# Kernel optimization log

Hardware: AMD Instinct MI355X
Metric: run time of the kernel (lower is better)

## Reference

```python
import jax, jax.numpy as jnp
import numpy as np

GRID_SIZE = 300


def setup_inputs() -> dict:
    key = jax.random.key(0)
    k1, k2 = jax.random.split(key)
    N, input_dim, out_dim = 2048, 256, 256
    x = jax.random.normal(k1, (N, input_dim), dtype=jnp.float32)
    scale = 1.0 / (np.sqrt(input_dim) * np.sqrt(GRID_SIZE))
    coeffs = jax.random.normal(k2, (2, out_dim, input_dim, GRID_SIZE), dtype=jnp.float32) * scale
    bias = jnp.zeros((1, out_dim), dtype=jnp.float32)
    return {"x": x, "coeffs": coeffs, "bias": bias}


def reference(x, coeffs, bias):
    # x: [N, I]; coeffs: [2, J, I, K]; bias: [1, J]
    grid_size = coeffs.shape[-1]
    k = jnp.arange(1, grid_size + 1, dtype=x.dtype)            # [K]
    ang = x[:, :, None] * k                                    # [N, I, K]
    c = jnp.cos(ang)
    s = jnp.sin(ang)
    # einsum('dbik,djik->bj') with d=2 split into cos/sin parts
    y = jnp.einsum('bik,jik->bj', c, coeffs[0]) + jnp.einsum('bik,jik->bj', s, coeffs[1])
    y = y + bias
    return y
```

## Files before the change

kernel.cpp:

```cpp
#include <hip/hip_runtime.h>
#include <stdint.h>

#define NB 2048
#define NI 256
#define NJ 256
#define GK 300
#define KPAD 320
#define KK_PER_I (2*KPAD)
#define NKC (NI*KK_PER_I/32)
#define CH_PER_I 20
#define SPLITK 32
#define II_PER_S (NI / SPLITK)
#define BM 128

#define B_BYTES  ((size_t)NKC * 16 * 1024)
#define P_BYTES  ((size_t)SPLITK * NB * NJ * 4)

typedef __bf16 bf16x8 __attribute__((ext_vector_type(8)));
typedef __bf16 bf16x2 __attribute__((ext_vector_type(2)));
typedef float  f32x4  __attribute__((ext_vector_type(4)));

__device__ __forceinline__ void sincos2pi(float ang, float& c, float& s) {
  float r = ang * 0.15915494309189535f;
  r = r - floorf(r);
  c = __builtin_amdgcn_cosf(r);
  s = __builtin_amdgcn_sinf(r);
}

__device__ __forceinline__ unsigned int pkbf(float c, float s) {
  bf16x2 p; p.x = (__bf16)c; p.y = (__bf16)s;
  return __builtin_bit_cast(unsigned int, p);
}

__device__ __forceinline__ void rot(float& c, float& s, float cr, float sr) {
  float nc = c * cr - s * sr;
  s = s * cr + c * sr;
  c = nc;
}

__global__ __launch_bounds__(256) void convert_b(const float* __restrict__ coeffs,
                                                 unsigned int* __restrict__ bw) {
  __shared__ uint4 sb[80][17];
  const int bid = blockIdx.x;
  const int i  = bid >> 4;
  const int jt = bid & 15;
  const int t  = (int)threadIdx.x;

  {
    const int jr = t >> 4;
    const int gq = t & 15;
    const int j  = jt * 16 + jr;
    const float4* r0 = (const float4*)(coeffs + (size_t)(j * NI + i) * GK);
    const float4* r1 = (const float4*)(coeffs + (size_t)((NJ + j) * NI + i) * GK);
    #pragma unroll
    for (int p = 0; p < 5; p++) {
      const int g = p * 16 + gq;
      uint4 w = {0u, 0u, 0u, 0u};
      if (g < GK / 4) {
        float4 a = r0[g];
        float4 b = r1[g];
        w.x = pkbf(a.x, b.x);
        w.y = pkbf(a.y, b.y);
        w.z = pkbf(a.z, b.z);
        w.w = pkbf(a.w, b.w);
      }
      sb[g][jr] = w;
    }
  }
  __syncthreads();
  {
    const int n  = t & 15;
    const int gl = t >> 4;
    #pragma unroll
    for (int p = 0; p < 5; p++) {
      const int g = p * 16 + gl;
      const int kc = i * 20 + (g >> 2);
      const unsigned int idx = ((unsigned int)(kc * 16 + jt) << 8) + ((g & 3) << 6) + (n << 2);
      *(uint4*)(bw + idx) = sb[g][n];
    }
  }
}

__global__ __launch_bounds__(256) void init_out(const float* __restrict__ bias,
                                                float* __restrict__ out) {
  const int tid = blockIdx.x * 256 + threadIdx.x;
  float4 b = ((const float4*)bias)[tid & 63];
  ((float4*)out)[tid] = b;
}

template <int MODE>
__global__ __launch_bounds__(256, 2) void fkan_gemm(const float* __restrict__ x,
                                                    const uint4* __restrict__ bw4,
                                                    float* __restrict__ dst) {
  const int bid  = blockIdx.x;
  const int virt = (bid & 7) * 64 + (bid >> 3);
  const int mt = virt & 15;
  const int s  = virt >> 4;
  const int m0 = mt * BM;

  const int t    = (int)threadIdx.x;
  const int lane = t & 63;
  const int wave = t >> 6;
  const int wr = wave >> 1;
  const int wc = wave & 1;
  const int q  = lane >> 4;
  const int ln = lane & 15;

  f32x4 acc[4][8];
  #pragma unroll
  for (int mm = 0; mm < 4; mm++)
    #pragma unroll
    for (int nn = 0; nn < 8; nn++)
      acc[mm][nn] = (f32x4){0.f, 0.f, 0.f, 0.f};

  const uint4* bptr = bw4 + (size_t)(wc * 8) * 64 + lane;

  int kc = s * (NKC / SPLITK);
  uint4 bcur[8], bnxt[8];
  #pragma unroll
  for (int nn = 0; nn < 8; nn++) bcur[nn] = bptr[(size_t)kc * 1024 + nn * 64];

  float stc[4], sts[4], c1a[4], s1a[4], cDa[4], sDa[4];

  #pragma unroll 1
  for (int ii = 0; ii < II_PER_S; ii++) {
    const int i = s * II_PER_S + ii;
    #pragma unroll
    for (int mm = 0; mm < 4; mm++) {
      const float xv = x[(m0 + wr * 64 + mm * 16 + ln) * NI + i];
      sincos2pi(xv, c1a[mm], s1a[mm]);
      sincos2pi(13.f * xv, cDa[mm], sDa[mm]);
      sincos2pi(xv * (float)(q * 4 + 1), stc[mm], sts[mm]);
    }

    #pragma unroll 2
    for (int c = 0; c < CH_PER_I; c++) {
      const int kcn = (kc + 1 < NKC) ? kc + 1 : kc;
      #pragma unroll
      for (int nn = 0; nn < 8; nn++)
        bnxt[nn] = bptr[(size_t)kcn * 1024 + nn * 64];

      bf16x8 af[4];
      #pragma unroll
      for (int mm = 0; mm < 4; mm++) {
        float cc = stc[mm], ss = sts[mm];
        uint4 u;
        u.x = pkbf(cc, ss);
        rot(cc, ss, c1a[mm], s1a[mm]); u.y = pkbf(cc, ss);
        rot(cc, ss, c1a[mm], s1a[mm]); u.z = pkbf(cc, ss);
        rot(cc, ss, c1a[mm], s1a[mm]); u.w = pkbf(cc, ss);
        rot(cc, ss, cDa[mm], sDa[mm]); stc[mm] = cc; sts[mm] = ss;
        af[mm] = __builtin_bit_cast(bf16x8, u);
      }

      #pragma unroll
      for (int nn = 0; nn < 8; nn++) {
        const bf16x8 bfr = __builtin_bit_cast(bf16x8, bcur[nn]);
        #pragma unroll
        for (int mm = 0; mm < 4; mm++)
          acc[mm][nn] = __builtin_amdgcn_mfma_f32_16x16x32_bf16(
              af[mm], bfr, acc[mm][nn], 0, 0, 0);
      }

      #pragma unroll
      for (int nn = 0; nn < 8; nn++) bcur[nn] = bnxt[nn];
      kc++;
    }
  }

  const int r0 = m0 + wr * 64 + q * 4;
  const int c0 = wc * 128 + ln;
  if (MODE == 0) {
    #pragma unroll
    for (int mm = 0; mm < 4; mm++)
      #pragma unroll
      for (int nn = 0; nn < 8; nn++)
        #pragma unroll
        for (int r = 0; r < 4; r++)
          atomicAdd(&dst[(r0 + mm * 16 + r) * NJ + c0 + nn * 16], acc[mm][nn][r]);
  } else {
    float* p = dst + (size_t)s * NB * NJ;
    #pragma unroll
    for (int mm = 0; mm < 4; mm++)
      #pragma unroll
      for (int nn = 0; nn < 8; nn++)
        #pragma unroll
        for (int r = 0; r < 4; r++)
          p[(r0 + mm * 16 + r) * NJ + c0 + nn * 16] = acc[mm][nn][r];
  }
}

__global__ __launch_bounds__(256) void reduce_out(const float* __restrict__ P,
                                                  const float* __restrict__ bias,
                                                  float* __restrict__ out) {
  const int m = blockIdx.x;
  const int j = (int)threadIdx.x;
  const size_t base = (size_t)m * NJ + j;
  float acc = bias[j];
  #pragma unroll
  for (int s = 0; s < SPLITK; s++)
    acc += P[(size_t)s * NB * NJ + base];
  out[base] = acc;
}

extern "C" void kernel_launch(void* const* d_in, const int* in_sizes, int n_in,
                              void* d_out, int out_size, void* d_ws, size_t ws_size,
                              hipStream_t stream) {
  const float* x      = (const float*)d_in[0];
  const float* coeffs = (const float*)d_in[1];
  const float* bias   = (const float*)d_in[2];
  float* out = (float*)d_out;
  unsigned int* bw = (unsigned int*)d_ws;

  convert_b<<<dim3(NI * 16), dim3(256), 0, stream>>>(coeffs, bw);

  if (ws_size >= B_BYTES + P_BYTES) {
    float* P = (float*)((char*)d_ws + B_BYTES);
    fkan_gemm<1><<<dim3(16 * SPLITK), dim3(256), 0, stream>>>(x, (const uint4*)bw, P);
    reduce_out<<<dim3(NB), dim3(256), 0, stream>>>(P, bias, out);
  } else {
    init_out<<<dim3(NB * NJ / 4 / 256), dim3(256), 0, stream>>>(bias, out);
    fkan_gemm<0><<<dim3(16 * SPLITK), dim3(256), 0, stream>>>(x, (const uint4*)bw, out);
  }
}
```

Before: 410.5 us.

## Fuse fp32-to-bf16 coefficient conversion into GEMM and drop the pre-pass

Removes the separate convert_b kernel, which repacked the fp32 coefficients into a bf16 tiled layout. The GEMM now reads the fp32 coeffs directly, converts them to packed bf16 in registers, and processes 19 chunks of 16 k per input feature instead of 20, zero-masking the tail. This saves one full read and write pass over the coefficients plus a kernel launch. In exchange the GEMM reads twice as many bytes from a strided, less coalesced layout, adds conversion ALU work, and each block converts the same coefficients again.

```diff
diff --git a/kernel.cpp b/kernel.cpp
--- a/kernel.cpp
+++ b/kernel.cpp
@@ -5,15 +5,13 @@
 #define NI 256
 #define NJ 256
 #define GK 300
-#define KPAD 320
-#define KK_PER_I (2*KPAD)
-#define NKC (NI*KK_PER_I/32)
-#define CH_PER_I 20
 #define SPLITK 32
 #define II_PER_S (NI / SPLITK)
 #define BM 128
-
-#define B_BYTES  ((size_t)NKC * 16 * 1024)
+#define CH 19
+#define ROW4 75
+#define SINOFF4 ((unsigned)(NJ * NI * ROW4))
+
 #define P_BYTES  ((size_t)SPLITK * NB * NJ * 4)
 
 typedef __bf16 bf16x8 __attribute__((ext_vector_type(8)));
@@ -38,49 +36,6 @@
   c = nc;
 }
 
-__global__ __launch_bounds__(256) void convert_b(const float* __restrict__ coeffs,
-                                                 unsigned int* __restrict__ bw) {
-  __shared__ uint4 sb[80][17];
-  const int bid = blockIdx.x;
-  const int i  = bid >> 4;
-  const int jt = bid & 15;
-  const int t  = (int)threadIdx.x;
-
-  {
-    const int jr = t >> 4;
-    const int gq = t & 15;
-    const int j  = jt * 16 + jr;
-    const float4* r0 = (const float4*)(coeffs + (size_t)(j * NI + i) * GK);
-    const float4* r1 = (const float4*)(coeffs + (size_t)((NJ + j) * NI + i) * GK);
-    #pragma unroll
-    for (int p = 0; p < 5; p++) {
-      const int g = p * 16 + gq;
-      uint4 w = {0u, 0u, 0u, 0u};
-      if (g < GK / 4) {
-        float4 a = r0[g];
-        float4 b = r1[g];
-        w.x = pkbf(a.x, b.x);
-        w.y = pkbf(a.y, b.y);
-        w.z = pkbf(a.z, b.z);
-        w.w = pkbf(a.w, b.w);
-      }
-      sb[g][jr] = w;
-    }
-  }
-  __syncthreads();
-  {
-    const int n  = t & 15;
-    const int gl = t >> 4;
-    #pragma unroll
-    for (int p = 0; p < 5; p++) {
-      const int g = p * 16 + gl;
-      const int kc = i * 20 + (g >> 2);
-      const unsigned int idx = ((unsigned int)(kc * 16 + jt) << 8) + ((g & 3) << 6) + (n << 2);
-      *(uint4*)(bw + idx) = sb[g][n];
-    }
-  }
-}
-
 __global__ __launch_bounds__(256) void init_out(const float* __restrict__ bias,
                                                 float* __restrict__ out) {
   const int tid = blockIdx.x * 256 + threadIdx.x;
@@ -90,7 +45,7 @@
 
 template <int MODE>
 __global__ __launch_bounds__(256, 2) void fkan_gemm(const float* __restrict__ x,
-                                                    const uint4* __restrict__ bw4,
+                                                    const float* __restrict__ coeffs,
                                                     float* __restrict__ dst) {
   const int bid  = blockIdx.x;
   const int virt = (bid & 7) * 64 + (bid >> 3);
@@ -106,6 +61,8 @@
   const int q  = lane >> 4;
   const int ln = lane & 15;
 
+  const float4* __restrict__ cf4 = (const float4*)coeffs;
+
   f32x4 acc[4][8];
   #pragma unroll
   for (int mm = 0; mm < 4; mm++)
@@ -113,18 +70,20 @@
     for (int nn = 0; nn < 8; nn++)
       acc[mm][nn] = (f32x4){0.f, 0.f, 0.f, 0.f};
 
-  const uint4* bptr = bw4 + (size_t)(wc * 8) * 64 + lane;
-
-  int kc = s * (NKC / SPLITK);
-  uint4 bcur[8], bnxt[8];
-  #pragma unroll
-  for (int nn = 0; nn < 8; nn++) bcur[nn] = bptr[(size_t)kc * 1024 + nn * 64];
-
   float stc[4], sts[4], c1a[4], s1a[4], cDa[4], sDa[4];
+  float4 f[8];
+  uint4  b[4];
+  bf16x8 af[4];
 
   #pragma unroll 1
   for (int ii = 0; ii < II_PER_S; ii++) {
     const int i = s * II_PER_S + ii;
+
+    unsigned idx[8];
+    #pragma unroll
+    for (int nn = 0; nn < 8; nn++)
+      idx[nn] = (unsigned)((((wc * 8 + nn) * 16 + ln) * NI + i)) * ROW4 + (unsigned)q;
+
     #pragma unroll
     for (int mm = 0; mm < 4; mm++) {
       const float xv = x[(m0 + wr * 64 + mm * 16 + ln) * NI + i];
@@ -133,14 +92,41 @@
       sincos2pi(xv * (float)(q * 4 + 1), stc[mm], sts[mm]);
     }
 
-    #pragma unroll 2
-    for (int c = 0; c < CH_PER_I; c++) {
-      const int kcn = (kc + 1 < NKC) ? kc + 1 : kc;
-      #pragma unroll
-      for (int nn = 0; nn < 8; nn++)
-        bnxt[nn] = bptr[(size_t)kcn * 1024 + nn * 64];
-
-      bf16x8 af[4];
+    #pragma unroll
+    for (int u = 0; u < 4; u++) {
+      const unsigned id = idx[u];
+      f[2*u]   = cf4[id];
+      f[2*u+1] = cf4[id + SINOFF4];
+    }
+
+    #pragma unroll 1
+    for (int c = 0; c < CH; c++) {
+      #pragma unroll
+      for (int u = 0; u < 4; u++) {
+        uint4 w;
+        w.x = pkbf(f[2*u].x, f[2*u+1].x);
+        w.y = pkbf(f[2*u].y, f[2*u+1].y);
+        w.z = pkbf(f[2*u].z, f[2*u+1].z);
+        w.w = pkbf(f[2*u].w, f[2*u+1].w);
+        b[u] = w;
+      }
+      if (c < CH - 1) {
+        #pragma unroll
+        for (int u = 0; u < 4; u++) {
+          const unsigned id = idx[4+u] + (unsigned)(c * 4);
+          f[2*u]   = cf4[id];
+          f[2*u+1] = cf4[id + SINOFF4];
+        }
+      } else {
+        const float4 zz = {0.f, 0.f, 0.f, 0.f};
+        #pragma unroll
+        for (int u = 0; u < 4; u++) {
+          const unsigned id = idx[4+u] + (unsigned)(c * 4);
+          f[2*u]   = (q < 3) ? cf4[id] : zz;
+          f[2*u+1] = (q < 3) ? cf4[id + SINOFF4] : zz;
+        }
+      }
+
       #pragma unroll
       for (int mm = 0; mm < 4; mm++) {
         float cc = stc[mm], ss = sts[mm];
@@ -154,17 +140,48 @@
       }
 
       #pragma unroll
-      for (int nn = 0; nn < 8; nn++) {
-        const bf16x8 bfr = __builtin_bit_cast(bf16x8, bcur[nn]);
+      for (int u = 0; u < 4; u++) {
+        const bf16x8 bfr = __builtin_bit_cast(bf16x8, b[u]);
         #pragma unroll
         for (int mm = 0; mm < 4; mm++)
-          acc[mm][nn] = __builtin_amdgcn_mfma_f32_16x16x32_bf16(
-              af[mm], bfr, acc[mm][nn], 0, 0, 0);
-      }
-
-      #pragma unroll
-      for (int nn = 0; nn < 8; nn++) bcur[nn] = bnxt[nn];
-      kc++;
+          acc[mm][u] = __builtin_amdgcn_mfma_f32_16x16x32_bf16(
+              af[mm], bfr, acc[mm][u], 0, 0, 0);
+      }
+
+      #pragma unroll
+      for (int u = 0; u < 4; u++) {
+        uint4 w;
+        w.x = pkbf(f[2*u].x, f[2*u+1].x);
+        w.y = pkbf(f[2*u].y, f[2*u+1].y);
+        w.z = pkbf(f[2*u].z, f[2*u+1].z);
+        w.w = pkbf(f[2*u].w, f[2*u+1].w);
+        b[u] = w;
+      }
+      if (c + 1 < CH - 1) {
+        #pragma unroll
+        for (int u = 0; u < 4; u++) {
+          const unsigned id = idx[u] + (unsigned)((c + 1) * 4);
+          f[2*u]   = cf4[id];
+          f[2*u+1] = cf4[id + SINOFF4];
+        }
+      } else if (c + 1 == CH - 1) {
+        const float4 zz = {0.f, 0.f, 0.f, 0.f};
+        #pragma unroll
+        for (int u = 0; u < 4; u++) {
+          const unsigned id = idx[u] + (unsigned)((c + 1) * 4);
+          f[2*u]   = (q < 3) ? cf4[id] : zz;
+          f[2*u+1] = (q < 3) ? cf4[id + SINOFF4] : zz;
+        }
+      }
+
+      #pragma unroll
+      for (int u = 0; u < 4; u++) {
+        const bf16x8 bfr = __builtin_bit_cast(bf16x8, b[u]);
+        #pragma unroll
+        for (int mm = 0; mm < 4; mm++)
+          acc[mm][4+u] = __builtin_amdgcn_mfma_f32_16x16x32_bf16(
+              af[mm], bfr, acc[mm][4+u], 0, 0, 0);
+      }
     }
   }
 
@@ -210,16 +227,13 @@
   const float* coeffs = (const float*)d_in[1];
   const float* bias   = (const float*)d_in[2];
   float* out = (float*)d_out;
-  unsigned int* bw = (unsigned int*)d_ws;
-
-  convert_b<<<dim3(NI * 16), dim3(256), 0, stream>>>(coeffs, bw);
-
-  if (ws_size >= B_BYTES + P_BYTES) {
-    float* P = (float*)((char*)d_ws + B_BYTES);
-    fkan_gemm<1><<<dim3(16 * SPLITK), dim3(256), 0, stream>>>(x, (const uint4*)bw, P);
+
+  if (ws_size >= P_BYTES) {
+    float* P = (float*)d_ws;
+    fkan_gemm<1><<<dim3(16 * SPLITK), dim3(256), 0, stream>>>(x, coeffs, P);
     reduce_out<<<dim3(NB), dim3(256), 0, stream>>>(P, bias, out);
   } else {
     init_out<<<dim3(NB * NJ / 4 / 256), dim3(256), 0, stream>>>(bias, out);
-    fkan_gemm<0><<<dim3(16 * SPLITK), dim3(256), 0, stream>>>(x, (const uint4*)bw, out);
+    fkan_gemm<0><<<dim3(16 * SPLITK), dim3(256), 0, stream>>>(x, coeffs, out);
   }
 }
```

Result: slower. 1.106 ms (+169.5%).
